# Optimization experiments

Hardware: AMD Instinct MI355X
Metric: run time of the kernel (lower is better)

## Reference

```python
import jax, jax.numpy as jnp
import numpy as np

N = 32768       # tokens
D_IN = 1024     # input_dim
D_OUT = 1024    # output_dim
E = 8           # num_experts
TOP_K = 2


def setup_inputs() -> dict:
    key = jax.random.key(0)
    k1, k2, k3, k4, k5 = jax.random.split(key, 5)
    scale = 1.0 / np.sqrt(D_IN)
    return {
        "x": jax.random.normal(k1, (N, D_IN), dtype=jnp.float32),
        "Wg": jax.random.uniform(k2, (E, D_IN), jnp.float32, -scale, scale),
        "bg": jax.random.uniform(k3, (E,), jnp.float32, -scale, scale),
        "W": jax.random.uniform(k4, (E, D_OUT, D_IN), jnp.float32, -scale, scale),
        "b": jax.random.uniform(k5, (E, D_OUT), jnp.float32, -scale, scale),
    }


def reference(x, Wg, bg, W, b):
    # Gating: softmax over experts, then top-k (weights NOT renormalized,
    # matching the original module).
    gate_scores = x @ Wg.T + bg                      # [N, E]
    gate_probs = jax.nn.softmax(gate_scores, axis=-1)
    topk_w, topk_idx = jax.lax.top_k(gate_probs, TOP_K)  # [N, K]

    # Per-token combine weight for each expert: sum_k w_k * onehot(idx_k)
    combine = (jax.nn.one_hot(topk_idx, E, dtype=x.dtype)
               * topk_w[..., None]).sum(axis=1)      # [N, E]

    # Dense per-expert GEMM + weighted combine (loop over small fixed E).
    out = jnp.zeros((x.shape[0], D_OUT), dtype=x.dtype)
    for e in range(E):
        out = out + combine[:, e:e + 1] * (x @ W[e].T + b[e])
    return out
```

## Files before the change

kernel.cpp:

```cpp
#include <hip/hip_runtime.h>
#include <hip/hip_bf16.h>
#include <cstdint>
#include <cstddef>

#define N_TOK   32768
#define D_IN    1024
#define D_OUT   1024
#define NE      8

typedef __attribute__((ext_vector_type(4))) float floatx4;
typedef __attribute__((ext_vector_type(8))) short bf16x8;

__device__ __forceinline__ unsigned short f2bf(float f) {
  union { float f; unsigned int u; } v; v.f = f;
  unsigned int u = v.u + 0x7fffu + ((v.u >> 16) & 1u);
  return (unsigned short)(u >> 16);
}

__device__ __forceinline__ void gload_lds16(const void* g, void* l) {
  __builtin_amdgcn_global_load_lds(
      (const __attribute__((address_space(1))) unsigned int*)g,
      (__attribute__((address_space(3))) unsigned int*)l, 16, 0, 0);
}

__global__ __launch_bounds__(256) void cast_w_kernel(const float* __restrict__ W,
                                                     unsigned short* __restrict__ Wb) {
  int i = blockIdx.x * 256 + threadIdx.x;
  float4 v = ((const float4*)W)[i];
  ushort4 h;
  h.x = f2bf(v.x); h.y = f2bf(v.y); h.z = f2bf(v.z); h.w = f2bf(v.w);
  ((ushort4*)Wb)[i] = h;
}

__global__ __launch_bounds__(256) void gate_kernel(
    const float* __restrict__ x,
    const float* __restrict__ Wg,
    const float* __restrict__ bg,
    unsigned short* __restrict__ xb,
    int* __restrict__ counts,
    int* __restrict__ bids,
    float* __restrict__ bw)
{
  __shared__ float wg_lds[NE * D_IN];
  __shared__ int lcnt[NE];
  __shared__ int basee[NE];
  __shared__ int   tok_e[64][2];
  __shared__ int   tok_s[64][2];
  __shared__ float tok_w[64][2];

  const int tid = threadIdx.x;
  {
    const float4* s = (const float4*)Wg;
    float4* d = (float4*)wg_lds;
    for (int i = tid; i < NE * D_IN / 4; i += 256) d[i] = s[i];
  }
  if (tid < NE) lcnt[tid] = 0;
  __syncthreads();

  const int wave = tid >> 6, lane = tid & 63;
  const float4* x4 = (const float4*)x;
  const float4* w4 = (const float4*)wg_lds;

  for (int t = 0; t < 16; ++t) {
    const int lt = wave * 16 + t;
    const int n  = blockIdx.x * 64 + lt;
    float4 xv[4];
    float acc[NE];
#pragma unroll
    for (int e = 0; e < NE; ++e) acc[e] = 0.f;
#pragma unroll
    for (int j = 0; j < 4; ++j) {
      xv[j] = x4[(size_t)n * 256 + j * 64 + lane];
#pragma unroll
      for (int e = 0; e < NE; ++e) {
        float4 w = w4[e * 256 + j * 64 + lane];
        acc[e] += xv[j].x * w.x + xv[j].y * w.y + xv[j].z * w.z + xv[j].w * w.w;
      }
    }
#pragma unroll
    for (int j = 0; j < 4; ++j) {
      ushort4 h;
      h.x = f2bf(xv[j].x); h.y = f2bf(xv[j].y);
      h.z = f2bf(xv[j].z); h.w = f2bf(xv[j].w);
      ((ushort4*)xb)[(size_t)n * 256 + j * 64 + lane] = h;
    }
#pragma unroll
    for (int e = 0; e < NE; ++e)
#pragma unroll
      for (int s = 32; s > 0; s >>= 1)
        acc[e] += __shfl_xor(acc[e], s, 64);

    if (lane == 0) {
      float sc[NE];
#pragma unroll
      for (int e = 0; e < NE; ++e) sc[e] = acc[e] + bg[e];
      float m = sc[0];
#pragma unroll
      for (int e = 1; e < NE; ++e) m = fmaxf(m, sc[e]);
      float p[NE], den = 0.f;
#pragma unroll
      for (int e = 0; e < NE; ++e) { p[e] = __expf(sc[e] - m); den += p[e]; }
      int e1 = 0;
#pragma unroll
      for (int e = 1; e < NE; ++e) if (sc[e] > sc[e1]) e1 = e;
      int e2 = (e1 == 0) ? 1 : 0;
#pragma unroll
      for (int e = 0; e < NE; ++e) if (e != e1 && sc[e] > sc[e2]) e2 = e;
      float inv = 1.f / den;
      tok_e[lt][0] = e1; tok_w[lt][0] = p[e1] * inv; tok_s[lt][0] = atomicAdd(&lcnt[e1], 1);
      tok_e[lt][1] = e2; tok_w[lt][1] = p[e2] * inv; tok_s[lt][1] = atomicAdd(&lcnt[e2], 1);
    }
  }
  __syncthreads();
  if (tid < NE) basee[tid] = atomicAdd(&counts[tid], lcnt[tid]);
  __syncthreads();
  if (tid < 128) {
    int lt = tid >> 1, kk = tid & 1;
    int e = tok_e[lt][kk];
    int slot = basee[e] + tok_s[lt][kk];
    bids[e * N_TOK + slot] = blockIdx.x * 64 + lt;
    bw[e * N_TOK + slot]   = tok_w[lt][kk];
  }
}

__global__ __launch_bounds__(256) void moe_gemm_kernel(
    const unsigned short* __restrict__ xb,
    const unsigned short* __restrict__ Wb,
    const float* __restrict__ bias,
    const int* __restrict__ counts,
    const int* __restrict__ bids,
    const float* __restrict__ bw,
    float* __restrict__ out)
{
  const int bid = blockIdx.x;
  const int e   = bid >> 11;
  const int mt  = (bid >> 3) & 255;
  const int nt  = bid & 7;
  const int cnt = counts[e];
  const int row0 = mt << 7;
  if (row0 >= cnt) return;
  const int rows = min(128, cnt - row0);

  __shared__ alignas(16) unsigned short Ald[128 * 32];
  __shared__ alignas(16) unsigned short Bld[128 * 32];
  __shared__ int   ids[128];
  __shared__ float wts[128];

  const int tid = threadIdx.x;
  if (tid < 128) {
    int src = (tid < rows) ? tid : 0;
    ids[tid] = bids[e * N_TOK + row0 + src];
    wts[tid] = (tid < rows) ? bw[e * N_TOK + row0 + tid] : 0.f;
  }
  __syncthreads();

  const int wave = tid >> 6;
  const int lane = tid & 63;
  const int wm = wave >> 1, wn = wave & 1;

  const int srow = lane >> 2;
  const int koff = (lane & 3) * 8;
  const int seg  = wave * 32;
  const long a_r0 = (long)ids[seg + srow] * D_IN;
  const long a_r1 = (long)ids[seg + 16 + srow] * D_IN;
  const unsigned short* wbe = Wb + (size_t)e * D_OUT * D_IN;
  const long b_r0 = (long)(nt * 128 + seg + srow) * D_IN;
  const long b_r1 = (long)(nt * 128 + seg + 16 + srow) * D_IN;
  unsigned short* aL0 = &Ald[seg * 32];
  unsigned short* aL1 = &Ald[(seg + 16) * 32];
  unsigned short* bL0 = &Bld[seg * 32];
  unsigned short* bL1 = &Bld[(seg + 16) * 32];

  const int m16  = lane & 15;
  const int quad = lane >> 4;

  floatx4 acc[4][4];
#pragma unroll
  for (int i = 0; i < 4; ++i)
#pragma unroll
    for (int j = 0; j < 4; ++j) acc[i][j] = (floatx4){0.f, 0.f, 0.f, 0.f};

  for (int k0 = 0; k0 < D_IN; k0 += 32) {
    gload_lds16(xb + a_r0 + k0 + koff, aL0);
    gload_lds16(xb + a_r1 + k0 + koff, aL1);
    gload_lds16(wbe + b_r0 + k0 + koff, bL0);
    gload_lds16(wbe + b_r1 + k0 + koff, bL1);
    __syncthreads();

    bf16x8 af[4], bf[4];
#pragma unroll
    for (int i = 0; i < 4; ++i)
      af[i] = *(const bf16x8*)&Ald[(wm * 64 + i * 16 + m16) * 32 + quad * 8];
#pragma unroll
    for (int j = 0; j < 4; ++j)
      bf[j] = *(const bf16x8*)&Bld[(wn * 64 + j * 16 + m16) * 32 + quad * 8];
#pragma unroll
    for (int i = 0; i < 4; ++i)
#pragma unroll
      for (int j = 0; j < 4; ++j)
        acc[i][j] = __builtin_amdgcn_mfma_f32_16x16x32_bf16(af[i], bf[j], acc[i][j], 0, 0, 0);
    __syncthreads();
  }

  float bv[4];
  int col[4];
#pragma unroll
  for (int j = 0; j < 4; ++j) {
    col[j] = nt * 128 + wn * 64 + j * 16 + m16;
    bv[j] = bias[e * D_OUT + col[j]];
  }
#pragma unroll
  for (int i = 0; i < 4; ++i) {
#pragma unroll
    for (int r = 0; r < 4; ++r) {
      int rl = wm * 64 + i * 16 + quad * 4 + r;
      if (rl < rows) {
        float w = wts[rl];
        float* orow = out + (size_t)ids[rl] * D_OUT;
#pragma unroll
        for (int j = 0; j < 4; ++j)
          atomicAdd(&orow[col[j]], w * (acc[i][j][r] + bv[j]));
      }
    }
  }
}

extern "C" void kernel_launch(void* const* d_in, const int* in_sizes, int n_in,
                              void* d_out, int out_size, void* d_ws, size_t ws_size,
                              hipStream_t stream) {
  const float* x  = (const float*)d_in[0];
  const float* Wg = (const float*)d_in[1];
  const float* bg = (const float*)d_in[2];
  const float* W  = (const float*)d_in[3];
  const float* b  = (const float*)d_in[4];
  float* out = (float*)d_out;

  char* ws = (char*)d_ws;
  int*   counts = (int*)ws;
  int*   bids   = (int*)(ws + 4096);
  float* bw     = (float*)(ws + 4096 + (size_t)NE * N_TOK * 4);
  unsigned short* xb = (unsigned short*)(ws + 4096 + (size_t)NE * N_TOK * 8);
  unsigned short* Wb = (unsigned short*)(ws + 4096 + (size_t)NE * N_TOK * 8 +
                                         (size_t)N_TOK * D_IN * 2);

  hipMemsetAsync(counts, 0, NE * sizeof(int), stream);
  hipMemsetAsync(out, 0, (size_t)out_size * sizeof(float), stream);

  cast_w_kernel<<<NE * D_OUT * D_IN / 1024, 256, 0, stream>>>(W, Wb);
  gate_kernel<<<N_TOK / 64, 256, 0, stream>>>(x, Wg, bg, xb, counts, bids, bw);
  moe_gemm_kernel<<<NE * 256 * 8, 256, 0, stream>>>(xb, Wb, b, counts, bids, bw, out);
}
```

Before: 618.2 us.

## Fuse weight cast, output zeroing and gating into one prep kernel; reorder GEMM grid

Merges the W bf16 cast, the output memset and the gate kernel into a single launch. Block ranges are partitioned by role: 512 blocks do gating, 512 do the cast and 2048 zero the output. This removes two launches and lets the three independent memory-bound jobs overlap. The GEMM block index is also remapped so that consecutive blocks cycle through experts and N tiles first. That spreads active tiles across experts early, with likely effects on load balance and cache locality.

Result: faster. 592.5 us (-4.2%).

```diff
diff --git a/kernel.cpp b/kernel.cpp
--- a/kernel.cpp
+++ b/kernel.cpp
@@ -23,23 +23,17 @@
       (__attribute__((address_space(3))) unsigned int*)l, 16, 0, 0);
 }
 
-__global__ __launch_bounds__(256) void cast_w_kernel(const float* __restrict__ W,
-                                                     unsigned short* __restrict__ Wb) {
-  int i = blockIdx.x * 256 + threadIdx.x;
-  float4 v = ((const float4*)W)[i];
-  ushort4 h;
-  h.x = f2bf(v.x); h.y = f2bf(v.y); h.z = f2bf(v.z); h.w = f2bf(v.w);
-  ((ushort4*)Wb)[i] = h;
-}
-
-__global__ __launch_bounds__(256) void gate_kernel(
+__global__ __launch_bounds__(256) void prep_kernel(
     const float* __restrict__ x,
     const float* __restrict__ Wg,
     const float* __restrict__ bg,
+    const float* __restrict__ W,
     unsigned short* __restrict__ xb,
+    unsigned short* __restrict__ Wb,
     int* __restrict__ counts,
     int* __restrict__ bids,
-    float* __restrict__ bw)
+    float* __restrict__ bw,
+    float* __restrict__ out)
 {
   __shared__ float wg_lds[NE * D_IN];
   __shared__ int lcnt[NE];
@@ -48,7 +42,31 @@
   __shared__ int   tok_s[64][2];
   __shared__ float tok_w[64][2];
 
+  const int blk = blockIdx.x;
   const int tid = threadIdx.x;
+
+  if (blk >= 1024) {
+    float4* o4 = (float4*)out;
+    const int base = (blk - 1024) * 4096;
+#pragma unroll
+    for (int i = 0; i < 16; ++i)
+      o4[base + i * 256 + tid] = (float4){0.f, 0.f, 0.f, 0.f};
+    return;
+  }
+  if (blk >= 512) {
+    const float4* s = (const float4*)W;
+    const int base = (blk - 512) * 4096;
+#pragma unroll
+    for (int i = 0; i < 16; ++i) {
+      int idx = base + i * 256 + tid;
+      float4 v = s[idx];
+      ushort4 h;
+      h.x = f2bf(v.x); h.y = f2bf(v.y); h.z = f2bf(v.z); h.w = f2bf(v.w);
+      ((ushort4*)Wb)[idx] = h;
+    }
+    return;
+  }
+
   {
     const float4* s = (const float4*)Wg;
     float4* d = (float4*)wg_lds;
@@ -63,7 +81,7 @@
 
   for (int t = 0; t < 16; ++t) {
     const int lt = wave * 16 + t;
-    const int n  = blockIdx.x * 64 + lt;
+    const int n  = blk * 64 + lt;
     float4 xv[4];
     float acc[NE];
 #pragma unroll
@@ -118,7 +136,7 @@
     int lt = tid >> 1, kk = tid & 1;
     int e = tok_e[lt][kk];
     int slot = basee[e] + tok_s[lt][kk];
-    bids[e * N_TOK + slot] = blockIdx.x * 64 + lt;
+    bids[e * N_TOK + slot] = blk * 64 + lt;
     bw[e * N_TOK + slot]   = tok_w[lt][kk];
   }
 }
@@ -133,9 +151,9 @@
     float* __restrict__ out)
 {
   const int bid = blockIdx.x;
-  const int e   = bid >> 11;
-  const int mt  = (bid >> 3) & 255;
-  const int nt  = bid & 7;
+  const int e   = bid & 7;
+  const int nt  = (bid >> 3) & 7;
+  const int mt  = bid >> 6;
   const int cnt = counts[e];
   const int row0 = mt << 7;
   if (row0 >= cnt) return;
@@ -244,9 +262,6 @@
                                          (size_t)N_TOK * D_IN * 2);
 
   hipMemsetAsync(counts, 0, NE * sizeof(int), stream);
-  hipMemsetAsync(out, 0, (size_t)out_size * sizeof(float), stream);
-
-  cast_w_kernel<<<NE * D_OUT * D_IN / 1024, 256, 0, stream>>>(W, Wb);
-  gate_kernel<<<N_TOK / 64, 256, 0, stream>>>(x, Wg, bg, xb, counts, bids, bw);
+  prep_kernel<<<3072, 256, 0, stream>>>(x, Wg, bg, W, xb, Wb, counts, bids, bw, out);
   moe_gemm_kernel<<<NE * 256 * 8, 256, 0, stream>>>(xb, Wb, b, counts, bids, bw, out);
 }
```
